# Performance work log

Hardware: AMD Instinct MI355X
Metric: run time of the kernel (lower is better)

Reference implementation:

```python
import jax, jax.numpy as jnp
import numpy as np

N, E, NC, F0, MID = 20000, 320000, 16, 67, 32
Y0 = 0.28209479177387814   # 1/(2*sqrt(pi)), real spherical harmonic l=0
C1 = 0.4886025119029199    # sqrt(3/(4*pi)),  real spherical harmonic l=1 coeff


def setup_inputs() -> dict:
    key = jax.random.key(0)
    ks = jax.random.split(key, 16)
    rn = lambda k, shape, s=1.0: jax.random.normal(k, shape, dtype=jnp.float32) * s
    return {
        "node_feats": rn(ks[0], (N, F0)),
        "pos": rn(ks[1], (N, 3)) * 3.0,
        "edge_w": jax.random.uniform(ks[2], (E, 2), dtype=jnp.float32),
        "lin1_W": rn(ks[5], (F0, F0), 1.0 / np.sqrt(F0)),
        "lin1_b": jnp.zeros((F0,), jnp.float32),
        "lin2_W": rn(ks[6], (F0, NC), 1.0 / np.sqrt(F0)),
        "lin2_b": jnp.zeros((NC,), jnp.float32),
        # 4 radial nets = 2 GConv layers x 2 degree pairs ((0,0),(0,1))
        "rW1": rn(ks[7], (4, 3, MID), 1.0 / np.sqrt(3)),
        "rb1": jnp.zeros((4, MID), jnp.float32),
        "ln1_g": jnp.ones((4, MID), jnp.float32),
        "ln1_b": jnp.zeros((4, MID), jnp.float32),
        "rW2": rn(ks[8], (4, MID, MID), 1.0 / np.sqrt(MID)),
        "rb2": jnp.zeros((4, MID), jnp.float32),
        "ln2_g": jnp.ones((4, MID), jnp.float32),
        "ln2_b": jnp.zeros((4, MID), jnp.float32),
        "rW3": rn(ks[9], (4, MID, NC * NC), 1.0 / np.sqrt(MID)),
        "rb3": jnp.zeros((4, NC * NC), jnp.float32),
        "Wself": rn(ks[10], (2, NC, NC), 1.0 / np.sqrt(NC)),
        "src": jax.random.randint(ks[3], (E,), 0, N),
        "dst": jax.random.randint(ks[4], (E,), 0, N),
    }


def _layer_norm(x, g, b, eps=1e-5):
    mu = jnp.mean(x, -1, keepdims=True)
    var = jnp.mean((x - mu) ** 2, -1, keepdims=True)
    return (x - mu) * jax.lax.rsqrt(var + eps) * g + b


def _forward(node_feats, pos, edge_w, lin1_W, lin1_b, lin2_W, lin2_b,
             rW1, rb1, ln1_g, ln1_b, rW2, rb2, ln2_g, ln2_b, rW3, rb3,
             Wself, src, dst):
    # node embedding: Linear -> ELU -> (dropout p=0) -> Linear -> [N, NC]
    h0 = jax.nn.elu(node_feats @ lin1_W + lin1_b) @ lin2_W + lin2_b

    # get_basis_and_r: relative positions, radial distance, SH basis (d_in=0)
    d = pos[dst] - pos[src]                                   # [E, 3]
    r = jnp.sqrt(jnp.sum(d * d, -1))                          # [E]
    rhat = d / jnp.maximum(r, 1e-8)[:, None]
    Y1 = C1 * rhat[:, jnp.array([1, 2, 0])]                   # [E, 3] (y, z, x order)
    feat = jnp.concatenate([edge_w, r[:, None]], -1)          # [E, edge_dim+1=3]

    deg = jax.ops.segment_sum(jnp.ones((E,), feat.dtype), dst, num_segments=N)
    inv_deg = jnp.where(deg > 0, 1.0 / jnp.maximum(deg, 1.0), 0.0)
    has_in = (deg > 0).astype(feat.dtype)

    def radial(i):
        h = jnp.maximum(_layer_norm(feat @ rW1[i] + rb1[i], ln1_g[i], ln1_b[i]), 0.0)
        h = jnp.maximum(_layer_norm(h @ rW2[i] + rb2[i], ln2_g[i], ln2_b[i]), 0.0)
        return (h @ rW3[i] + rb3[i]).reshape(E, NC, NC)       # [E, nc_out, nc_in]

    out1 = None
    for li in range(2):  # faithful to source bug: both layers read only degree-0 feats
        R00 = radial(2 * li)        # pairwise kernel (0->0), num_freq=1
        R01 = radial(2 * li + 1)    # pairwise kernel (0->1), num_freq=1
        s = h0[src]                                           # [E, NC] gather
        msg0 = Y0 * jnp.einsum('eoi,ei->eo', R00, s)          # [E, NC]
        msg1 = jnp.einsum('eoi,ei,em->eom', R01, s, Y1)       # [E, NC, 3]
        out0 = jax.ops.segment_sum(msg0, dst, num_segments=N) * inv_deg[:, None]
        out0 = out0 + has_in[:, None] * (h0 @ Wself[li].T)    # self-interaction (deg 0)
        out1 = jax.ops.segment_sum(msg1, dst, num_segments=N) * inv_deg[:, None, None]
        h0 = out0
    return h0[:, :, None], out1                               # {'0': [N,NC,1], '1': [N,NC,3]}


def reference(node_feats, pos, edge_w, lin1_W, lin1_b, lin2_W, lin2_b,
              rW1, rb1, ln1_g, ln1_b, rW2, rb2, ln2_g, ln2_b, rW3, rb3,
              Wself, src, dst):
    return _forward(node_feats, pos, edge_w, lin1_W, lin1_b, lin2_W, lin2_b,
                    rW1, rb1, ln1_g, ln1_b, rW2, rb2, ln2_g, ln2_b, rW3, rb3,
                    Wself, src, dst)
```

## Files before the change

kernel.cpp:

```cpp
#include <hip/hip_runtime.h>
#include <hip/hip_fp16.h>


#define Y0C 0.28209479177387814f
#define C1C 0.4886025119029199f

typedef _Float16 hv2 __attribute__((ext_vector_type(2)));

#if defined(__has_builtin)
#if __has_builtin(__builtin_amdgcn_fdot2)
#define FDOT2(a, b, c) __builtin_amdgcn_fdot2((a), (b), (c), false)
#endif
#endif
#ifndef FDOT2
#define FDOT2(a, b, c) ((c) + (float)(a).x * (float)(b).x + (float)(a).y * (float)(b).y)
#endif

static __device__ __forceinline__ unsigned h2u(__half2 h) {
    union { __half2 h; unsigned u; } x; x.h = h; return x.u;
}
static __device__ __forceinline__ __half2 u2h(unsigned u) {
    union { unsigned u; __half2 h; } x; x.u = u; return x.h;
}
static __device__ __forceinline__ hv2 u2hv(unsigned u) {
    union { unsigned u; hv2 h; } x; x.u = u; return x.h;
}
static __device__ __forceinline__ unsigned hv2u(hv2 h) {
    union { hv2 h; unsigned u; } x; x.h = h; return x.u;
}
static __device__ __forceinline__ hv2 f2hv(float a, float b) {
    hv2 r; r.x = (_Float16)a; r.y = (_Float16)b; return r;
}
static __device__ __forceinline__ float hbits2f(unsigned short s) {
    __half_raw r; r.x = s; return __half2float((__half)r);
}

struct RadialW {
    const float *W1, *b1, *g1, *gb1, *b2, *g2, *gb2;
    const unsigned* W2q;
};

__device__ __forceinline__ void radial_net_pk(float x0, float x1, float x2,
                                              RadialW rw, hv2* hvpk ) {
    float h[32];
#pragma unroll
    for (int j = 0; j < 32; ++j)
        h[j] = rw.b1[j] + x0 * rw.W1[j] + x1 * rw.W1[32 + j] + x2 * rw.W1[64 + j];
    float mu = 0.f;
#pragma unroll
    for (int j = 0; j < 32; ++j) mu += h[j];
    mu *= 0.03125f;
    float var = 0.f;
#pragma unroll
    for (int j = 0; j < 32; ++j) { float d = h[j] - mu; var += d * d; }
    var *= 0.03125f;
    float rs = rsqrtf(var + 1e-5f);
#pragma unroll
    for (int j = 0; j < 32; ++j)
        h[j] = fmaxf((h[j] - mu) * rs * rw.g1[j] + rw.gb1[j], 0.f);

    hv2 hp[16];
#pragma unroll
    for (int p = 0; p < 16; ++p) hp[p] = f2hv(h[2 * p], h[2 * p + 1]);

    float h2[32];
#pragma unroll
    for (int j = 0; j < 32; ++j) {
        float acc = rw.b2[j];
        const unsigned* __restrict__ wj = rw.W2q + j * 16;
#pragma unroll
        for (int kp = 0; kp < 16; ++kp)
            acc = FDOT2(hp[kp], u2hv(wj[kp]), acc);
        h2[j] = acc;
    }
    mu = 0.f;
#pragma unroll
    for (int j = 0; j < 32; ++j) mu += h2[j];
    mu *= 0.03125f;
    var = 0.f;
#pragma unroll
    for (int j = 0; j < 32; ++j) { float d = h2[j] - mu; var += d * d; }
    var *= 0.03125f;
    rs = rsqrtf(var + 1e-5f);
    float y[32];
#pragma unroll
    for (int j = 0; j < 32; ++j)
        y[j] = fmaxf((h2[j] - mu) * rs * rw.g2[j] + rw.gb2[j], 0.f);
#pragma unroll
    for (int p = 0; p < 16; ++p) hvpk[p] = f2hv(y[2 * p], y[2 * p + 1]);
}

__device__ __forceinline__ void contract_dot(const hv2* hvpk,
                                             const uint4* __restrict__ Um,
                                             const float* __restrict__ Ut,
                                             float* v ) {
    float4 t0 = ((const float4*)Ut)[0];
    float4 t1 = ((const float4*)Ut)[1];
    float4 t2 = ((const float4*)Ut)[2];
    float4 t3 = ((const float4*)Ut)[3];
    float tail[16] = {t0.x, t0.y, t0.z, t0.w, t1.x, t1.y, t1.z, t1.w,
                      t2.x, t2.y, t2.z, t2.w, t3.x, t3.y, t3.z, t3.w};
#pragma unroll
    for (int o = 0; o < 16; ++o) {
        uint4 q0 = Um[o * 4];
        uint4 q1 = Um[o * 4 + 1];
        uint4 q2 = Um[o * 4 + 2];
        uint4 q3 = Um[o * 4 + 3];
        float acc = tail[o];
        acc = FDOT2(hvpk[0],  u2hv(q0.x), acc);
        acc = FDOT2(hvpk[1],  u2hv(q0.y), acc);
        acc = FDOT2(hvpk[2],  u2hv(q0.z), acc);
        acc = FDOT2(hvpk[3],  u2hv(q0.w), acc);
        acc = FDOT2(hvpk[4],  u2hv(q1.x), acc);
        acc = FDOT2(hvpk[5],  u2hv(q1.y), acc);
        acc = FDOT2(hvpk[6],  u2hv(q1.z), acc);
        acc = FDOT2(hvpk[7],  u2hv(q1.w), acc);
        acc = FDOT2(hvpk[8],  u2hv(q2.x), acc);
        acc = FDOT2(hvpk[9],  u2hv(q2.y), acc);
        acc = FDOT2(hvpk[10], u2hv(q2.z), acc);
        acc = FDOT2(hvpk[11], u2hv(q2.w), acc);
        acc = FDOT2(hvpk[12], u2hv(q3.x), acc);
        acc = FDOT2(hvpk[13], u2hv(q3.y), acc);
        acc = FDOT2(hvpk[14], u2hv(q3.z), acc);
        acc = FDOT2(hvpk[15], u2hv(q3.w), acc);
        v[o] = acc;
    }
}

__global__ void k_embed1(const float* __restrict__ nf, const float* __restrict__ W1,
                         const float* __restrict__ b1, float* __restrict__ t, int N) {
    int idx = blockIdx.x * blockDim.x + threadIdx.x;
    if (idx >= N * 67) return;
    int n = idx / 67, j = idx - n * 67;
    const float* __restrict__ x = nf + (size_t)n * 67;
    float s = b1[j];
    for (int i = 0; i < 67; ++i) s += x[i] * W1[i * 67 + j];
    t[idx] = (s > 0.f) ? s : expm1f(s);
}

__global__ void k_embed2(const float* __restrict__ t, const float* __restrict__ W2,
                         const float* __restrict__ b2, float* __restrict__ h0, int N) {
    int idx = blockIdx.x * blockDim.x + threadIdx.x;
    if (idx >= N * 16) return;
    int n = idx >> 4, c = idx & 15;
    const float* __restrict__ x = t + (size_t)n * 67;
    float s = b2[c];
    for (int i = 0; i < 67; ++i) s += x[i] * W2[i * 16 + c];
    h0[idx] = s;
}

__global__ void k_count2(const int* __restrict__ src, const int* __restrict__ dst,
                         int* __restrict__ cntd, int* __restrict__ cnts,
                         int* __restrict__ posd, int* __restrict__ poss, int E) {
    int e = blockIdx.x * blockDim.x + threadIdx.x;
    if (e >= E) return;
    posd[e] = atomicAdd(cntd + dst[e], 1);
    poss[e] = atomicAdd(cnts + src[e], 1);
}

__global__ __launch_bounds__(1024) void k_scan2(const int* __restrict__ cntd,
                                                int* __restrict__ rsd,
                                                const int* __restrict__ cnts,
                                                int* __restrict__ rss, int N) {
    const int* __restrict__ c = (blockIdx.x == 0) ? cntd : cnts;
    int* __restrict__ rs      = (blockIdx.x == 0) ? rsd  : rss;
    int chunk = (N + 1023) >> 10;
    int lo = (int)threadIdx.x * chunk;
    int sum = 0;
    for (int j = 0; j < chunk; ++j) { int i = lo + j; sum += (i < N) ? c[i] : 0; }
    __shared__ int ps[1024];
    ps[threadIdx.x] = sum;
    __syncthreads();
    for (int off = 1; off < 1024; off <<= 1) {
        int t = (threadIdx.x >= (unsigned)off) ? ps[threadIdx.x - off] : 0;
        __syncthreads();
        ps[threadIdx.x] += t;
        __syncthreads();
    }
    int run = threadIdx.x ? ps[threadIdx.x - 1] : 0;
    if (threadIdx.x == 0) rs[0] = 0;
    for (int j = 0; j < chunk; ++j) {
        int i = lo + j;
        if (i < N) { run += c[i]; rs[i + 1] = run; }
    }
}

__global__ void k_prep(const float* __restrict__ pos, const float* __restrict__ ew,
                       const int* __restrict__ src, const int* __restrict__ dst,
                       const int* __restrict__ rsd, const int* __restrict__ rss,
                       const int* __restrict__ posd, const int* __restrict__ poss,
                       float4* __restrict__ edgeS, uint2* __restrict__ y1d,
                       int* __restrict__ s2d, int E) {
    int e = blockIdx.x * blockDim.x + threadIdx.x;
    if (e >= E) return;
    int s = src[e], d = dst[e];
    float dx = pos[3 * d]     - pos[3 * s];
    float dy = pos[3 * d + 1] - pos[3 * s + 1];
    float dz = pos[3 * d + 2] - pos[3 * s + 2];
    float r = sqrtf(dx * dx + dy * dy + dz * dz);
    float im = 1.f / fmaxf(r, 1e-8f);
    int ts = rss[s] + poss[e];
    int td = rsd[d] + posd[e];
    s2d[ts] = td;
    edgeS[ts] = make_float4(ew[2 * e], ew[2 * e + 1], r, __int_as_float(s));
    y1d[td] = make_uint2(h2u(__floats2half2_rn(C1C * dy * im, C1C * dz * im)),
                         h2u(__floats2half2_rn(C1C * dx * im, 0.f)));
}

__global__ void k_pack(const float* __restrict__ rW3, const float* __restrict__ rW2,
                       unsigned* __restrict__ Wp, unsigned* __restrict__ Wq) {
    int t = blockIdx.x * blockDim.x + threadIdx.x;
    if (t < 3 * 256) {
        int ni = t >> 8;
        int net = (ni == 0) ? 0 : ni + 1;
        int r = t & 255;
        int i = r >> 4, o = r & 15;
        const float* __restrict__ W3n = rW3 + (size_t)net * 8192;
        unsigned* __restrict__ dp = Wp + (size_t)ni * 4608 + (size_t)(i * 16 + o) * 18;
#pragma unroll
        for (int kp = 0; kp < 16; ++kp) {
            float a = W3n[(2 * kp) * 256 + o * 16 + i];
            float b = W3n[(2 * kp + 1) * 256 + o * 16 + i];
            dp[kp] = h2u(__floats2half2_rn(a, b));
        }
    } else if (t < 3 * 256 + 3 * 512) {
        int r = t - 3 * 256;
        int ni = r / 512;
        int net = (ni == 0) ? 0 : ni + 1;
        int jk = r - ni * 512;
        int j = jk >> 4, kp = jk & 15;
        const float* __restrict__ W2n = rW2 + (size_t)net * 1024;
        Wq[ni * 512 + j * 16 + kp] =
            h2u(__floats2half2_rn(W2n[(2 * kp) * 32 + j], W2n[(2 * kp + 1) * 32 + j]));
    }
}

__global__ __launch_bounds__(256) void k_u2(
    const float* __restrict__ h, const unsigned* __restrict__ Wp,
    const float* __restrict__ b3A, const float* __restrict__ b3B,
    unsigned* __restrict__ Um0, float* __restrict__ Ut0,
    unsigned* __restrict__ Um1, float* __restrict__ Ut1,
    int wpA, int nbPerNet, int N) {
    __shared__ unsigned WL[4608];
    int netSel = blockIdx.x / nbPerNet;
    int nbase = (blockIdx.x - netSel * nbPerNet) * 32;
    const unsigned* __restrict__ g = Wp + (size_t)(wpA + netSel) * 4608;
    for (int j = threadIdx.x; j < 4608; j += 256) WL[j] = g[j];
    __syncthreads();

    const float* __restrict__ b3 = netSel ? b3B : b3A;
    unsigned* __restrict__ Um = netSel ? Um1 : Um0;
    float*    __restrict__ Ut = netSel ? Ut1 : Ut0;

    int o = threadIdx.x & 15;
    int pr = threadIdx.x >> 4;
    int n0 = nbase + pr * 2;
    int n1 = n0 + 1;
    bool ok0 = n0 < N, ok1 = n1 < N;
    int m0 = ok0 ? n0 : 0, m1 = ok1 ? n1 : 0;

    const float* __restrict__ bo = b3 + o * 16;
    float tA = 0.f, tB = 0.f;
    __half2 hhA[16], hhB[16];
    {
        const float4* hp = (const float4*)(h + (size_t)m0 * 16);
#pragma unroll
        for (int q = 0; q < 4; ++q) {
            float4 hv = hp[q];
            tA += hv.x * bo[4 * q] + hv.y * bo[4 * q + 1]
                + hv.z * bo[4 * q + 2] + hv.w * bo[4 * q + 3];
            hhA[4 * q]     = __floats2half2_rn(hv.x, hv.x);
            hhA[4 * q + 1] = __floats2half2_rn(hv.y, hv.y);
            hhA[4 * q + 2] = __floats2half2_rn(hv.z, hv.z);
            hhA[4 * q + 3] = __floats2half2_rn(hv.w, hv.w);
        }
    }
    {
        const float4* hp = (const float4*)(h + (size_t)m1 * 16);
#pragma unroll
        for (int q = 0; q < 4; ++q) {
            float4 hv = hp[q];
            tB += hv.x * bo[4 * q] + hv.y * bo[4 * q + 1]
                + hv.z * bo[4 * q + 2] + hv.w * bo[4 * q + 3];
            hhB[4 * q]     = __floats2half2_rn(hv.x, hv.x);
            hhB[4 * q + 1] = __floats2half2_rn(hv.y, hv.y);
            hhB[4 * q + 2] = __floats2half2_rn(hv.z, hv.z);
            hhB[4 * q + 3] = __floats2half2_rn(hv.w, hv.w);
        }
    }

    __half2 accA[16], accB[16];
#pragma unroll
    for (int p = 0; p < 16; ++p) {
        accA[p] = __floats2half2_rn(0.f, 0.f);
        accB[p] = __floats2half2_rn(0.f, 0.f);
    }

#pragma unroll
    for (int i = 0; i < 16; ++i) {
        const uint2* __restrict__ row = (const uint2*)(WL + i * 288 + o * 18);
        __half2 ha = hhA[i], hb = hhB[i];
#pragma unroll
        for (int q = 0; q < 8; ++q) {
            uint2 w = row[q];
            accA[2 * q]     = __hfma2(ha, u2h(w.x), accA[2 * q]);
            accA[2 * q + 1] = __hfma2(ha, u2h(w.y), accA[2 * q + 1]);
            accB[2 * q]     = __hfma2(hb, u2h(w.x), accB[2 * q]);
            accB[2 * q + 1] = __hfma2(hb, u2h(w.y), accB[2 * q + 1]);
        }
    }

    if (ok0) {
        uint4* du = (uint4*)(Um + ((size_t)(n0 * 16 + o)) * 16);
#pragma unroll
        for (int q = 0; q < 4; ++q)
            du[q] = make_uint4(h2u(accA[4 * q]), h2u(accA[4 * q + 1]),
                               h2u(accA[4 * q + 2]), h2u(accA[4 * q + 3]));
        Ut[n0 * 16 + o] = tA;
    }
    if (ok1) {
        uint4* du = (uint4*)(Um + ((size_t)(n1 * 16 + o)) * 16);
#pragma unroll
        for (int q = 0; q < 4; ++q)
            du[q] = make_uint4(h2u(accB[4 * q]), h2u(accB[4 * q + 1]),
                               h2u(accB[4 * q + 2]), h2u(accB[4 * q + 3]));
        Ut[n1 * 16 + o] = tB;
    }
}

__global__ __launch_bounds__(256) void k_edgeL0(
    const float4* __restrict__ edgeS, const int* __restrict__ s2d, RadialW ra,
    const uint4* __restrict__ UmA, const float* __restrict__ UtA,
    unsigned short* __restrict__ msg , int E) {
    int t = blockIdx.x * blockDim.x + threadIdx.x;
    if (t >= E) return;
    float4 a = edgeS[t];
    int sn = __float_as_int(a.w);
    hv2 hv[16];
    float v[16];
    radial_net_pk(a.x, a.y, a.z, ra, hv);
    contract_dot(hv, UmA + (size_t)sn * 64, UtA + (size_t)sn * 16, v);
    int td = s2d[t];
    uint4* m = (uint4*)(msg + (size_t)td * 16);
    m[0] = make_uint4(hv2u(f2hv(v[0], v[1])),  hv2u(f2hv(v[2], v[3])),
                      hv2u(f2hv(v[4], v[5])),  hv2u(f2hv(v[6], v[7])));
    m[1] = make_uint4(hv2u(f2hv(v[8], v[9])),  hv2u(f2hv(v[10], v[11])),
                      hv2u(f2hv(v[12], v[13])), hv2u(f2hv(v[14], v[15])));
}

__global__ __launch_bounds__(256) void k_edgeL1(
    const float4* __restrict__ edgeS, const int* __restrict__ s2d,
    RadialW ra, RadialW rb,
    const uint4* __restrict__ UmA, const float* __restrict__ UtA,
    const uint4* __restrict__ UmB, const float* __restrict__ UtB,
    unsigned short* __restrict__ msg , int nbE, int E) {
    int half = (blockIdx.x >= (unsigned)nbE) ? 1 : 0;
    int t = (blockIdx.x - half * nbE) * blockDim.x + threadIdx.x;
    if (t >= E) return;
    float4 a = edgeS[t];
    int sn = __float_as_int(a.w);
    RadialW rw = half ? rb : ra;
    const uint4* __restrict__ Um = half ? UmB : UmA;
    const float* __restrict__ Ut = half ? UtB : UtA;
    hv2 hv[16];
    float v[16];
    radial_net_pk(a.x, a.y, a.z, rw, hv);
    contract_dot(hv, Um + (size_t)sn * 64, Ut + (size_t)sn * 16, v);
    int td = s2d[t];
    uint4* m = (uint4*)(msg + (size_t)td * 32 + half * 16);
    m[0] = make_uint4(hv2u(f2hv(v[0], v[1])),  hv2u(f2hv(v[2], v[3])),
                      hv2u(f2hv(v[4], v[5])),  hv2u(f2hv(v[6], v[7])));
    m[1] = make_uint4(hv2u(f2hv(v[8], v[9])),  hv2u(f2hv(v[10], v[11])),
                      hv2u(f2hv(v[12], v[13])), hv2u(f2hv(v[14], v[15])));
}

__global__ void k_reduce0(const unsigned short* __restrict__ msg,
                          const int* __restrict__ rowstart,
                          const float* __restrict__ h, const float* __restrict__ Wself,
                          float* __restrict__ out, int N) {
    int idx = blockIdx.x * blockDim.x + threadIdx.x;
    if (idx >= N * 16) return;
    int n = idx >> 4, o = idx & 15;
    int s = rowstart[n], t1 = rowstart[n + 1];
    float acc = 0.f;
    for (int t = s; t < t1; ++t) acc += hbits2f(msg[(size_t)t * 16 + o]);
    int d = t1 - s;
    float invd = (d > 0) ? 1.f / (float)d : 0.f;
    float hi   = (d > 0) ? 1.f : 0.f;
    const float* __restrict__ hn = h + (size_t)n * 16;
    const float* __restrict__ w  = Wself + o * 16;
    float self = 0.f;
#pragma unroll
    for (int c = 0; c < 16; ++c) self += hn[c] * w[c];
    out[idx] = Y0C * acc * invd + hi * self;
}

__global__ void k_reduce1(const unsigned short* __restrict__ msg,
                          const uint2* __restrict__ y1d,
                          const int* __restrict__ rowstart,
                          const float* __restrict__ h, const float* __restrict__ Wself,
                          float* __restrict__ out0, float* __restrict__ out1, int N) {
    int idx = blockIdx.x * blockDim.x + threadIdx.x;
    if (idx >= N * 16) return;
    int n = idx >> 4, o = idx & 15;
    int s = rowstart[n], t1 = rowstart[n + 1];
    float a0 = 0.f, ax = 0.f, ay = 0.f, az = 0.f;
    for (int t = s; t < t1; ++t) {
        const unsigned short* row = msg + (size_t)t * 32;
        a0 += hbits2f(row[o]);
        float b = hbits2f(row[16 + o]);
        uint2 yv = y1d[t];
        ax += b * hbits2f((unsigned short)yv.x);
        ay += b * hbits2f((unsigned short)(yv.x >> 16));
        az += b * hbits2f((unsigned short)yv.y);
    }
    int d = t1 - s;
    float invd = (d > 0) ? 1.f / (float)d : 0.f;
    float hi   = (d > 0) ? 1.f : 0.f;
    const float* __restrict__ hn = h + (size_t)n * 16;
    const float* __restrict__ w  = Wself + o * 16;
    float self = 0.f;
#pragma unroll
    for (int c = 0; c < 16; ++c) self += hn[c] * w[c];
    out0[idx] = Y0C * a0 * invd + hi * self;
    out1[(size_t)idx * 3]     = ax * invd;
    out1[(size_t)idx * 3 + 1] = ay * invd;
    out1[(size_t)idx * 3 + 2] = az * invd;
}

extern "C" void kernel_launch(void* const* d_in, const int* in_sizes, int n_in,
                              void* d_out, int out_size, void* d_ws, size_t ws_size,
                              hipStream_t stream) {
    (void)n_in; (void)out_size; (void)ws_size;
    const float* node_feats = (const float*)d_in[0];
    const float* pos    = (const float*)d_in[1];
    const float* edge_w = (const float*)d_in[2];
    const float* lin1_W = (const float*)d_in[3];
    const float* lin1_b = (const float*)d_in[4];
    const float* lin2_W = (const float*)d_in[5];
    const float* lin2_b = (const float*)d_in[6];
    const float* rW1    = (const float*)d_in[7];
    const float* rb1    = (const float*)d_in[8];
    const float* ln1_g  = (const float*)d_in[9];
    const float* ln1_b  = (const float*)d_in[10];
    const float* rW2    = (const float*)d_in[11];
    const float* rb2    = (const float*)d_in[12];
    const float* ln2_g  = (const float*)d_in[13];
    const float* ln2_b  = (const float*)d_in[14];
    const float* rW3    = (const float*)d_in[15];
    const float* rb3    = (const float*)d_in[16];
    const float* Wself  = (const float*)d_in[17];
    const int*   src    = (const int*)d_in[18];
    const int*   dst    = (const int*)d_in[19];

    const int N = in_sizes[1] / 3;
    const int E = in_sizes[18];

    char* ws = (char*)d_ws;
    size_t off = 0;
    auto carve = [&](size_t bytes) -> char* {
        char* p = ws + off;
        off = (off + bytes + 255) & ~(size_t)255;
        return p;
    };
    float* h0   = (float*)carve((size_t)N * 16 * 4);
    float* h1   = (float*)carve((size_t)N * 16 * 4);
    int*   cntd = (int*)carve((size_t)N * 4);
    int*   cnts = (int*)carve((size_t)N * 4);
    int*   rsd  = (int*)carve((size_t)(N + 1) * 4);
    int*   rss  = (int*)carve((size_t)(N + 1) * 4);
    int*   s2d  = (int*)carve((size_t)E * 4);
    float4* edgeS = (float4*)carve((size_t)E * 16);
    uint2*  y1d   = (uint2*)carve((size_t)E * 8);
    unsigned* UaM = (unsigned*)carve((size_t)N * 16 * 64);
    float*    UaT = (float*)carve((size_t)N * 16 * 4);
    unsigned* UbM = (unsigned*)carve((size_t)N * 16 * 64);
    float*    UbT = (float*)carve((size_t)N * 16 * 4);
    unsigned* Wp  = (unsigned*)carve((size_t)3 * 4608 * 4);
    unsigned* Wq  = (unsigned*)carve((size_t)3 * 512 * 4);
    unsigned short* msg = (unsigned short*)carve((size_t)E * 32 * 2);
    float* tmb  = (float*)msg;
    int*   posd = (int*)((char*)msg + (8u << 20));
    int*   poss = (int*)((char*)msg + (14u << 20));

    auto nb = [](int n) { return (n + 255) / 256; };
    const int nbE = nb(E);
    const int nbU = (N + 31) / 32;

    hipMemsetAsync(cntd, 0, (size_t)((char*)cnts - (char*)cntd) + (size_t)N * 4, stream);

    k_pack<<<nb(3 * 256 + 3 * 512), 256, 0, stream>>>(rW3, rW2, Wp, Wq);
    k_embed1<<<nb(N * 67), 256, 0, stream>>>(node_feats, lin1_W, lin1_b, tmb, N);
    k_embed2<<<nb(N * 16), 256, 0, stream>>>(tmb, lin2_W, lin2_b, h0, N);

    k_count2<<<nbE, 256, 0, stream>>>(src, dst, cntd, cnts, posd, poss, E);
    k_scan2<<<2, 1024, 0, stream>>>(cntd, rsd, cnts, rss, N);
    k_prep<<<nbE, 256, 0, stream>>>(pos, edge_w, src, dst, rsd, rss, posd, poss,
                                    edgeS, y1d, s2d, E);

    auto rnet = [&](int net, int ni) -> RadialW {
        RadialW r;
        r.W1 = rW1 + net * 96;   r.b1 = rb1 + net * 32;
        r.g1 = ln1_g + net * 32; r.gb1 = ln1_b + net * 32;
        r.b2 = rb2 + net * 32;
        r.g2 = ln2_g + net * 32; r.gb2 = ln2_b + net * 32;
        r.W2q = Wq + ni * 512;
        return r;
    };

    k_u2<<<nbU, 256, 0, stream>>>(h0, Wp, rb3, rb3, UaM, UaT, UbM, UbT,
                                  0, nbU, N);
    k_edgeL0<<<nbE, 256, 0, stream>>>(edgeS, s2d, rnet(0, 0), (const uint4*)UaM, UaT,
                                      msg, E);
    k_reduce0<<<nb(N * 16), 256, 0, stream>>>(msg, rsd, h0, Wself, h1, N);

    k_u2<<<2 * nbU, 256, 0, stream>>>(h1, Wp, rb3 + 2 * 256, rb3 + 3 * 256,
                                      UaM, UaT, UbM, UbT, 1, nbU, N);
    k_edgeL1<<<2 * nbE, 256, 0, stream>>>(edgeS, s2d, rnet(2, 1), rnet(3, 2),
                                          (const uint4*)UaM, UaT,
                                          (const uint4*)UbM, UbT, msg, nbE, E);
    float* out0 = (float*)d_out;
    float* out1 = (float*)d_out + (size_t)N * 16;
    k_reduce1<<<nb(N * 16), 256, 0, stream>>>(msg, y1d, rsd, h1, Wself + 256,
                                              out0, out1, N);
}
```

Before: 360.7 us.

## Fuse embedding MLP with weight packing and add multi-accumulator reductions

Merges the two embedding kernels and the weight-packing kernel into one launch, with one wavefront per node that stages features and the hidden layer in shared memory. This removes the intermediate global buffer and two launches. Layer-norm mean and variance reductions in the radial net and the segment-sum gather loops are also split across several independent accumulators to shorten dependency chains. Splitting the accumulators changes the floating-point summation order slightly.

Measured after the change: 355.6 us. About the same (-1.4%).

```diff
diff --git a/kernel.cpp b/kernel.cpp
--- a/kernel.cpp
+++ b/kernel.cpp
@@ -46,14 +46,21 @@
 #pragma unroll
     for (int j = 0; j < 32; ++j)
         h[j] = rw.b1[j] + x0 * rw.W1[j] + x1 * rw.W1[32 + j] + x2 * rw.W1[64 + j];
-    float mu = 0.f;
-#pragma unroll
-    for (int j = 0; j < 32; ++j) mu += h[j];
-    mu *= 0.03125f;
-    float var = 0.f;
-#pragma unroll
-    for (int j = 0; j < 32; ++j) { float d = h[j] - mu; var += d * d; }
-    var *= 0.03125f;
+    float s0 = 0.f, s1 = 0.f, s2 = 0.f, s3 = 0.f;
+#pragma unroll
+    for (int p = 0; p < 8; ++p) {
+        s0 += h[4 * p]; s1 += h[4 * p + 1]; s2 += h[4 * p + 2]; s3 += h[4 * p + 3];
+    }
+    float mu = ((s0 + s1) + (s2 + s3)) * 0.03125f;
+    float v0 = 0.f, v1 = 0.f, v2 = 0.f, v3 = 0.f;
+#pragma unroll
+    for (int p = 0; p < 8; ++p) {
+        float d0 = h[4 * p] - mu, d1 = h[4 * p + 1] - mu;
+        float d2 = h[4 * p + 2] - mu, d3 = h[4 * p + 3] - mu;
+        v0 = fmaf(d0, d0, v0); v1 = fmaf(d1, d1, v1);
+        v2 = fmaf(d2, d2, v2); v3 = fmaf(d3, d3, v3);
+    }
+    float var = ((v0 + v1) + (v2 + v3)) * 0.03125f;
     float rs = rsqrtf(var + 1e-5f);
 #pragma unroll
     for (int j = 0; j < 32; ++j)
@@ -73,14 +80,21 @@
             acc = FDOT2(hp[kp], u2hv(wj[kp]), acc);
         h2[j] = acc;
     }
-    mu = 0.f;
-#pragma unroll
-    for (int j = 0; j < 32; ++j) mu += h2[j];
-    mu *= 0.03125f;
-    var = 0.f;
-#pragma unroll
-    for (int j = 0; j < 32; ++j) { float d = h2[j] - mu; var += d * d; }
-    var *= 0.03125f;
+    s0 = s1 = s2 = s3 = 0.f;
+#pragma unroll
+    for (int p = 0; p < 8; ++p) {
+        s0 += h2[4 * p]; s1 += h2[4 * p + 1]; s2 += h2[4 * p + 2]; s3 += h2[4 * p + 3];
+    }
+    mu = ((s0 + s1) + (s2 + s3)) * 0.03125f;
+    v0 = v1 = v2 = v3 = 0.f;
+#pragma unroll
+    for (int p = 0; p < 8; ++p) {
+        float d0 = h2[4 * p] - mu, d1 = h2[4 * p + 1] - mu;
+        float d2 = h2[4 * p + 2] - mu, d3 = h2[4 * p + 3] - mu;
+        v0 = fmaf(d0, d0, v0); v1 = fmaf(d1, d1, v1);
+        v2 = fmaf(d2, d2, v2); v3 = fmaf(d3, d3, v3);
+    }
+    var = ((v0 + v1) + (v2 + v3)) * 0.03125f;
     rs = rsqrtf(var + 1e-5f);
     float y[32];
 #pragma unroll
@@ -127,26 +141,70 @@
     }
 }
 
-__global__ void k_embed1(const float* __restrict__ nf, const float* __restrict__ W1,
-                         const float* __restrict__ b1, float* __restrict__ t, int N) {
-    int idx = blockIdx.x * blockDim.x + threadIdx.x;
-    if (idx >= N * 67) return;
-    int n = idx / 67, j = idx - n * 67;
-    const float* __restrict__ x = nf + (size_t)n * 67;
-    float s = b1[j];
-    for (int i = 0; i < 67; ++i) s += x[i] * W1[i * 67 + j];
-    t[idx] = (s > 0.f) ? s : expm1f(s);
-}
-
-__global__ void k_embed2(const float* __restrict__ t, const float* __restrict__ W2,
-                         const float* __restrict__ b2, float* __restrict__ h0, int N) {
-    int idx = blockIdx.x * blockDim.x + threadIdx.x;
-    if (idx >= N * 16) return;
-    int n = idx >> 4, c = idx & 15;
-    const float* __restrict__ x = t + (size_t)n * 67;
-    float s = b2[c];
-    for (int i = 0; i < 67; ++i) s += x[i] * W2[i * 16 + c];
-    h0[idx] = s;
+__global__ __launch_bounds__(256) void k_embed_pack(
+    const float* __restrict__ nf, const float* __restrict__ W1,
+    const float* __restrict__ b1, const float* __restrict__ W2,
+    const float* __restrict__ b2, float* __restrict__ h0, int N, int nbEmb,
+    const float* __restrict__ rW3, const float* __restrict__ rW2,
+    unsigned* __restrict__ Wp, unsigned* __restrict__ Wq) {
+    if (blockIdx.x >= (unsigned)nbEmb) {
+        int t = (blockIdx.x - nbEmb) * 256 + threadIdx.x;
+        if (t < 3 * 256) {
+            int ni = t >> 8;
+            int net = (ni == 0) ? 0 : ni + 1;
+            int r = t & 255;
+            int i = r >> 4, o = r & 15;
+            const float* __restrict__ W3n = rW3 + (size_t)net * 8192;
+            unsigned* __restrict__ dp = Wp + (size_t)ni * 4608 + (size_t)(i * 16 + o) * 18;
+#pragma unroll
+            for (int kp = 0; kp < 16; ++kp) {
+                float a = W3n[(2 * kp) * 256 + o * 16 + i];
+                float b = W3n[(2 * kp + 1) * 256 + o * 16 + i];
+                dp[kp] = h2u(__floats2half2_rn(a, b));
+            }
+        } else if (t < 3 * 256 + 3 * 512) {
+            int r = t - 3 * 256;
+            int ni = r / 512;
+            int net = (ni == 0) ? 0 : ni + 1;
+            int jk = r - ni * 512;
+            int j = jk >> 4, kp = jk & 15;
+            const float* __restrict__ W2n = rW2 + (size_t)net * 1024;
+            Wq[ni * 512 + j * 16 + kp] =
+                h2u(__floats2half2_rn(W2n[(2 * kp) * 32 + j],
+                                      W2n[(2 * kp + 1) * 32 + j]));
+        }
+        return;
+    }
+    __shared__ float xs[4][68];
+    __shared__ float ts[4][68];
+    int w = threadIdx.x >> 6, lane = threadIdx.x & 63;
+    int n = blockIdx.x * 4 + w;
+    bool ok = n < N;
+    int nn = ok ? n : (N - 1);
+    const float* __restrict__ x = nf + (size_t)nn * 67;
+    xs[w][lane] = x[lane];
+    if (lane < 3) xs[w][64 + lane] = x[64 + lane];
+    __syncthreads();
+    int j2 = 64 + lane; int j2c = (j2 < 67) ? j2 : 66;
+    float a0 = b1[lane], a1 = b1[j2c];
+    for (int i = 0; i < 67; ++i) {
+        float xi = xs[w][i];
+        a0 = fmaf(xi, W1[i * 67 + lane], a0);
+        a1 = fmaf(xi, W1[i * 67 + j2c], a1);
+    }
+    ts[w][lane] = (a0 > 0.f) ? a0 : expm1f(a0);
+    if (lane < 3) ts[w][64 + lane] = (a1 > 0.f) ? a1 : expm1f(a1);
+    __syncthreads();
+    int c = lane & 15, q = lane >> 4;
+    int i0 = q * 17, i1 = (i0 + 17 < 67) ? (i0 + 17) : 67;
+    float s = (q == 0) ? b2[c] : 0.f;
+    for (int i = i0; i < i1; ++i) s = fmaf(ts[w][i], W2[i * 16 + c], s);
+    __syncthreads();
+    xs[w][lane] = s;
+    __syncthreads();
+    if (ok && lane < 16)
+        h0[(size_t)n * 16 + lane] =
+            (xs[w][lane] + xs[w][lane + 16]) + (xs[w][lane + 32] + xs[w][lane + 48]);
 }
 
 __global__ void k_count2(const int* __restrict__ src, const int* __restrict__ dst,
@@ -205,34 +263,6 @@
     edgeS[ts] = make_float4(ew[2 * e], ew[2 * e + 1], r, __int_as_float(s));
     y1d[td] = make_uint2(h2u(__floats2half2_rn(C1C * dy * im, C1C * dz * im)),
                          h2u(__floats2half2_rn(C1C * dx * im, 0.f)));
-}
-
-__global__ void k_pack(const float* __restrict__ rW3, const float* __restrict__ rW2,
-                       unsigned* __restrict__ Wp, unsigned* __restrict__ Wq) {
-    int t = blockIdx.x * blockDim.x + threadIdx.x;
-    if (t < 3 * 256) {
-        int ni = t >> 8;
-        int net = (ni == 0) ? 0 : ni + 1;
-        int r = t & 255;
-        int i = r >> 4, o = r & 15;
-        const float* __restrict__ W3n = rW3 + (size_t)net * 8192;
-        unsigned* __restrict__ dp = Wp + (size_t)ni * 4608 + (size_t)(i * 16 + o) * 18;
-#pragma unroll
-        for (int kp = 0; kp < 16; ++kp) {
-            float a = W3n[(2 * kp) * 256 + o * 16 + i];
-            float b = W3n[(2 * kp + 1) * 256 + o * 16 + i];
-            dp[kp] = h2u(__floats2half2_rn(a, b));
-        }
-    } else if (t < 3 * 256 + 3 * 512) {
-        int r = t - 3 * 256;
-        int ni = r / 512;
-        int net = (ni == 0) ? 0 : ni + 1;
-        int jk = r - ni * 512;
-        int j = jk >> 4, kp = jk & 15;
-        const float* __restrict__ W2n = rW2 + (size_t)net * 1024;
-        Wq[ni * 512 + j * 16 + kp] =
-            h2u(__floats2half2_rn(W2n[(2 * kp) * 32 + j], W2n[(2 * kp + 1) * 32 + j]));
-    }
 }
 
 __global__ __launch_bounds__(256) void k_u2(
@@ -382,8 +412,14 @@
     if (idx >= N * 16) return;
     int n = idx >> 4, o = idx & 15;
     int s = rowstart[n], t1 = rowstart[n + 1];
-    float acc = 0.f;
-    for (int t = s; t < t1; ++t) acc += hbits2f(msg[(size_t)t * 16 + o]);
+    float acc0 = 0.f, acc1 = 0.f;
+    int t = s;
+    for (; t + 1 < t1; t += 2) {
+        acc0 += hbits2f(msg[(size_t)t * 16 + o]);
+        acc1 += hbits2f(msg[(size_t)(t + 1) * 16 + o]);
+    }
+    if (t < t1) acc0 += hbits2f(msg[(size_t)t * 16 + o]);
+    float acc = acc0 + acc1;
     int d = t1 - s;
     float invd = (d > 0) ? 1.f / (float)d : 0.f;
     float hi   = (d > 0) ? 1.f : 0.f;
@@ -405,15 +441,34 @@
     int n = idx >> 4, o = idx & 15;
     int s = rowstart[n], t1 = rowstart[n + 1];
     float a0 = 0.f, ax = 0.f, ay = 0.f, az = 0.f;
-    for (int t = s; t < t1; ++t) {
-        const unsigned short* row = msg + (size_t)t * 32;
-        a0 += hbits2f(row[o]);
-        float b = hbits2f(row[16 + o]);
-        uint2 yv = y1d[t];
-        ax += b * hbits2f((unsigned short)yv.x);
-        ay += b * hbits2f((unsigned short)(yv.x >> 16));
-        az += b * hbits2f((unsigned short)yv.y);
-    }
+    float b0 = 0.f, bx = 0.f, by = 0.f, bz = 0.f;
+    int t = s;
+    for (; t + 1 < t1; t += 2) {
+        const unsigned short* rowA = msg + (size_t)t * 32;
+        const unsigned short* rowB = msg + (size_t)(t + 1) * 32;
+        uint2 yva = y1d[t];
+        uint2 yvb = y1d[t + 1];
+        a0 += hbits2f(rowA[o]);
+        b0 += hbits2f(rowB[o]);
+        float pa = hbits2f(rowA[16 + o]);
+        float pb = hbits2f(rowB[16 + o]);
+        ax = fmaf(pa, hbits2f((unsigned short)yva.x), ax);
+        ay = fmaf(pa, hbits2f((unsigned short)(yva.x >> 16)), ay);
+        az = fmaf(pa, hbits2f((unsigned short)yva.y), az);
+        bx = fmaf(pb, hbits2f((unsigned short)yvb.x), bx);
+        by = fmaf(pb, hbits2f((unsigned short)(yvb.x >> 16)), by);
+        bz = fmaf(pb, hbits2f((unsigned short)yvb.y), bz);
+    }
+    if (t < t1) {
+        const unsigned short* rowA = msg + (size_t)t * 32;
+        uint2 yva = y1d[t];
+        a0 += hbits2f(rowA[o]);
+        float pa = hbits2f(rowA[16 + o]);
+        ax = fmaf(pa, hbits2f((unsigned short)yva.x), ax);
+        ay = fmaf(pa, hbits2f((unsigned short)(yva.x >> 16)), ay);
+        az = fmaf(pa, hbits2f((unsigned short)yva.y), az);
+    }
+    a0 += b0; ax += bx; ay += by; az += bz;
     int d = t1 - s;
     float invd = (d > 0) ? 1.f / (float)d : 0.f;
     float hi   = (d > 0) ? 1.f : 0.f;
@@ -479,19 +534,19 @@
     unsigned* Wp  = (unsigned*)carve((size_t)3 * 4608 * 4);
     unsigned* Wq  = (unsigned*)carve((size_t)3 * 512 * 4);
     unsigned short* msg = (unsigned short*)carve((size_t)E * 32 * 2);
-    float* tmb  = (float*)msg;
-    int*   posd = (int*)((char*)msg + (8u << 20));
-    int*   poss = (int*)((char*)msg + (14u << 20));
+    int* posd = (int*)((char*)msg + (8u << 20));
+    int* poss = (int*)((char*)msg + (14u << 20));
 
     auto nb = [](int n) { return (n + 255) / 256; };
     const int nbE = nb(E);
     const int nbU = (N + 31) / 32;
+    const int nbEmb = (N + 3) / 4;
 
     hipMemsetAsync(cntd, 0, (size_t)((char*)cnts - (char*)cntd) + (size_t)N * 4, stream);
 
-    k_pack<<<nb(3 * 256 + 3 * 512), 256, 0, stream>>>(rW3, rW2, Wp, Wq);
-    k_embed1<<<nb(N * 67), 256, 0, stream>>>(node_feats, lin1_W, lin1_b, tmb, N);
-    k_embed2<<<nb(N * 16), 256, 0, stream>>>(tmb, lin2_W, lin2_b, h0, N);
+    k_embed_pack<<<nbEmb + 9, 256, 0, stream>>>(node_feats, lin1_W, lin1_b,
+                                                lin2_W, lin2_b, h0, N, nbEmb,
+                                                rW3, rW2, Wp, Wq);
 
     k_count2<<<nbE, 256, 0, stream>>>(src, dst, cntd, cnts, posd, poss, E);
     k_scan2<<<2, 1024, 0, stream>>>(cntd, rsd, cnts, rss, N);
```
